# Performance work log

Measured on AMD Instinct MI355X. Metric: run time of the kernel, lower is better.

Reference implementation:

```python
import jax, jax.numpy as jnp
import numpy as np

N_ATOMS = 100000   # 'i' axis: atoms/edges
N_CHAN = 128       # 'f' axis: channel multiplicity
DIM_L1 = 3         # 2*l1+1, l1=1
DIM_L2 = 3         # 2*l2+1, l2=1
DIM_L3 = 5         # 2*l3+1, l3=2


def setup_inputs() -> dict:
    key = jax.random.key(0)
    kx, ky, kc = jax.random.split(key, 3)
    x = jax.random.normal(kx, (N_ATOMS, N_CHAN, DIM_L1), dtype=jnp.float32)
    y = jax.random.normal(ky, (N_ATOMS, N_CHAN, DIM_L2), dtype=jnp.float32)
    cgc = jax.random.normal(kc, (DIM_L1, DIM_L2, DIM_L3), dtype=jnp.float32)
    return {"x": x, "y": y, "cgc": cgc}


def reference(x, y, cgc):
    # Clebsch-Gordan tensor product contraction:
    # res[i,f,h] = sum_{m,n} cgc[m,n,h] * x[i,f,m] * y[i,f,n]
    return jnp.einsum('mnh,ifm,ifn->ifh', cgc, x, y)
```

## Files before the change

### kernel.cpp

```cpp
#include <hip/hip_runtime.h>


constexpr int N_PAIRS = 100000 * 128;
constexpr int PAIRS_PER_BLOCK = 1024;
constexpr int NBLOCKS = N_PAIRS / PAIRS_PER_BLOCK;

__global__ __launch_bounds__(256) void tp_contract_kernel(
    const float* __restrict__ x,
    const float* __restrict__ y,
    const float* __restrict__ cgc,
    float* __restrict__ out)
{
    __shared__ float4 smem[1536];

    const int tid = threadIdx.x;
    const size_t blk = blockIdx.x;

    float c[3][3][5];
#pragma unroll
    for (int m = 0; m < 3; ++m)
#pragma unroll
        for (int n = 0; n < 3; ++n)
#pragma unroll
            for (int h = 0; h < 5; ++h)
                c[m][n][h] = cgc[(m * 3 + n) * 5 + h];

    const float4* gx = reinterpret_cast<const float4*>(x) + blk * 768;
    const float4* gy = reinterpret_cast<const float4*>(y) + blk * 768;
#pragma unroll
    for (int j = 0; j < 3; ++j) {
        smem[j * 256 + tid]       = gx[j * 256 + tid];
        smem[768 + j * 256 + tid] = gy[j * 256 + tid];
    }
    __syncthreads();

    float4 xv0 = smem[tid * 3 + 0];
    float4 xv1 = smem[tid * 3 + 1];
    float4 xv2 = smem[tid * 3 + 2];
    float4 yv0 = smem[768 + tid * 3 + 0];
    float4 yv1 = smem[768 + tid * 3 + 1];
    float4 yv2 = smem[768 + tid * 3 + 2];

    float xs[12] = { xv0.x, xv0.y, xv0.z, xv0.w,
                     xv1.x, xv1.y, xv1.z, xv1.w,
                     xv2.x, xv2.y, xv2.z, xv2.w };
    float ys[12] = { yv0.x, yv0.y, yv0.z, yv0.w,
                     yv1.x, yv1.y, yv1.z, yv1.w,
                     yv2.x, yv2.y, yv2.z, yv2.w };

    float o[20];
#pragma unroll
    for (int p = 0; p < 4; ++p) {
        float acc[5] = {0.f, 0.f, 0.f, 0.f, 0.f};
#pragma unroll
        for (int m = 0; m < 3; ++m) {
#pragma unroll
            for (int n = 0; n < 3; ++n) {
                const float xy = xs[p * 3 + m] * ys[p * 3 + n];
#pragma unroll
                for (int h = 0; h < 5; ++h)
                    acc[h] = fmaf(c[m][n][h], xy, acc[h]);
            }
        }
#pragma unroll
        for (int h = 0; h < 5; ++h) o[p * 5 + h] = acc[h];
    }

    __syncthreads();

#pragma unroll
    for (int q = 0; q < 5; ++q)
        smem[tid * 5 + q] = make_float4(o[q * 4 + 0], o[q * 4 + 1],
                                        o[q * 4 + 2], o[q * 4 + 3]);
    __syncthreads();

    float4* go = reinterpret_cast<float4*>(out) + blk * 1280;
#pragma unroll
    for (int j = 0; j < 5; ++j)
        go[j * 256 + tid] = smem[j * 256 + tid];
}

extern "C" void kernel_launch(void* const* d_in, const int* in_sizes, int n_in,
                              void* d_out, int out_size, void* d_ws, size_t ws_size,
                              hipStream_t stream) {
    const float* x   = (const float*)d_in[0];
    const float* y   = (const float*)d_in[1];
    const float* cgc = (const float*)d_in[2];
    float* out = (float*)d_out;

    tp_contract_kernel<<<NBLOCKS, 256, 0, stream>>>(x, y, cgc, out);
}
```

Before: 105.9 us.

## Use direct global-to-LDS loads, per-wave output staging, and nontemporal stores

Input loads now use the AMDGCN global_load_lds builtin, which writes global data straight into shared memory without passing through registers. The output staging is reorganised so each wave writes and reads back only its own region of shared memory, reusing the slots that held its x and y inputs. This removes the two block-wide barriers around the output transpose. Results are written with nontemporal stores to avoid polluting the cache. The change relies on wave-private LDS regions being safe without a barrier, and on the 16-byte global_load_lds form being supported on this target.

Measured after the change: 93.27 us. 11.9% less time.

```diff
diff --git a/kernel.cpp b/kernel.cpp
--- a/kernel.cpp
+++ b/kernel.cpp
@@ -1,9 +1,12 @@
 #include <hip/hip_runtime.h>
+#include <string.h>
 
 
 constexpr int N_PAIRS = 100000 * 128;
 constexpr int PAIRS_PER_BLOCK = 1024;
 constexpr int NBLOCKS = N_PAIRS / PAIRS_PER_BLOCK;
+
+typedef float vf4 __attribute__((ext_vector_type(4)));
 
 __global__ __launch_bounds__(256) void tp_contract_kernel(
     const float* __restrict__ x,
@@ -13,7 +16,9 @@
 {
     __shared__ float4 smem[1536];
 
-    const int tid = threadIdx.x;
+    const int tid  = threadIdx.x;
+    const int lane = tid & 63;
+    const int w    = tid >> 6;
     const size_t blk = blockIdx.x;
 
     float c[3][3][5];
@@ -29,8 +34,14 @@
     const float4* gy = reinterpret_cast<const float4*>(y) + blk * 768;
 #pragma unroll
     for (int j = 0; j < 3; ++j) {
-        smem[j * 256 + tid]       = gx[j * 256 + tid];
-        smem[768 + j * 256 + tid] = gy[j * 256 + tid];
+        __builtin_amdgcn_global_load_lds(
+            (const __attribute__((address_space(1))) void*)(gx + j * 256 + w * 64 + lane),
+            (__attribute__((address_space(3))) void*)(&smem[j * 256 + w * 64]),
+            16, 0, 0);
+        __builtin_amdgcn_global_load_lds(
+            (const __attribute__((address_space(1))) void*)(gy + j * 256 + w * 64 + lane),
+            (__attribute__((address_space(3))) void*)(&smem[768 + j * 256 + w * 64]),
+            16, 0, 0);
     }
     __syncthreads();
 
@@ -66,18 +77,26 @@
         for (int h = 0; h < 5; ++h) o[p * 5 + h] = acc[h];
     }
 
-    __syncthreads();
+#pragma unroll
+    for (int q = 0; q < 5; ++q) {
+        const int oidx = lane * 5 + q;
+        const int a = (oidx < 192) ? (w * 192 + oidx)
+                                   : (768 + w * 192 + (oidx - 192));
+        smem[a] = make_float4(o[q * 4 + 0], o[q * 4 + 1],
+                              o[q * 4 + 2], o[q * 4 + 3]);
+    }
 
+    float4* go = reinterpret_cast<float4*>(out) + blk * 1280 + (size_t)w * 320;
 #pragma unroll
-    for (int q = 0; q < 5; ++q)
-        smem[tid * 5 + q] = make_float4(o[q * 4 + 0], o[q * 4 + 1],
-                                        o[q * 4 + 2], o[q * 4 + 3]);
-    __syncthreads();
-
-    float4* go = reinterpret_cast<float4*>(out) + blk * 1280;
-#pragma unroll
-    for (int j = 0; j < 5; ++j)
-        go[j * 256 + tid] = smem[j * 256 + tid];
+    for (int j = 0; j < 5; ++j) {
+        const int oidx = j * 64 + lane;
+        const int a = (oidx < 192) ? (w * 192 + oidx)
+                                   : (768 + w * 192 + (oidx - 192));
+        float4 v = smem[a];
+        vf4 vv;
+        memcpy(&vv, &v, 16);
+        __builtin_nontemporal_store(vv, reinterpret_cast<vf4*>(&go[j * 64 + lane]));
+    }
 }
 
 extern "C" void kernel_launch(void* const* d_in, const int* in_sizes, int n_in,
```
